# Performance work log

Measured on AMD Instinct MI355X. Metric: run time of the kernel, lower is better.

Reference implementation:

```python
import jax, jax.numpy as jnp
import numpy as np

N_NODES = 100000
N_EDGES = 1600000
IN_CH = 128
HID = 128
BN_EPS = 1e-5


def setup_inputs() -> dict:
    key = jax.random.key(0)
    ks = jax.random.split(key, 16)
    x = jax.random.normal(ks[0], (N_NODES, IN_CH), dtype=jnp.float32)
    edge_index = jax.random.randint(ks[1], (2, N_EDGES), 0, N_NODES, dtype=jnp.int32)
    edge_attr = jax.random.uniform(ks[2], (N_EDGES,), dtype=jnp.float32)
    def glorot(k, fan_in, fan_out):
        s = jnp.sqrt(6.0 / (fan_in + fan_out))
        return jax.random.uniform(k, (fan_in, fan_out), dtype=jnp.float32, minval=-s, maxval=s)
    W1 = glorot(ks[3], IN_CH, HID)
    b1 = jnp.zeros((HID,), jnp.float32)
    gamma1 = jnp.ones((HID,), jnp.float32)
    beta1 = jnp.zeros((HID,), jnp.float32)
    W2 = glorot(ks[4], HID, HID)
    b2 = jnp.zeros((HID,), jnp.float32)
    gamma2 = jnp.ones((HID,), jnp.float32)
    beta2 = jnp.zeros((HID,), jnp.float32)
    W3 = glorot(ks[5], HID, 1)
    b3 = jnp.zeros((1,), jnp.float32)
    return {"x": x, "edge_index": edge_index, "edge_attr": edge_attr,
            "W1": W1, "b1": b1, "gamma1": gamma1, "beta1": beta1,
            "W2": W2, "b2": b2, "gamma2": gamma2, "beta2": beta2,
            "W3": W3, "b3": b3}


def _gcn_norm(edge_index, edge_weight, num_nodes):
    # PyG gcn_norm with add_self_loops=True, self-loop weight 1.0
    sl = jnp.arange(num_nodes, dtype=edge_index.dtype)
    row = jnp.concatenate([edge_index[0], sl])  # source
    col = jnp.concatenate([edge_index[1], sl])  # target
    w = jnp.concatenate([edge_weight, jnp.ones((num_nodes,), edge_weight.dtype)])
    deg = jax.ops.segment_sum(w, col, num_segments=num_nodes)
    dinv = jnp.where(deg > 0, jax.lax.rsqrt(jnp.maximum(deg, 1e-30)), 0.0)
    norm = dinv[row] * w * dinv[col]
    return row, col, norm


def _gcn_conv(x, W, b, row, col, norm, num_nodes):
    xw = x @ W                       # [N, out]
    msg = xw[row] * norm[:, None]    # gather + scale, [E+N, out]
    out = jax.ops.segment_sum(msg, col, num_segments=num_nodes)  # scatter-add
    return out + b


def _batchnorm(x, gamma, beta):
    mean = jnp.mean(x, axis=0)
    var = jnp.mean(jnp.square(x - mean), axis=0)  # biased var (torch BN)
    return (x - mean) * jax.lax.rsqrt(var + BN_EPS) * gamma + beta


def reference(x, edge_index, edge_attr, W1, b1, gamma1, beta1, W2, b2, gamma2, beta2, W3, b3):
    n = x.shape[0]
    row, col, norm = _gcn_norm(edge_index, edge_attr, n)
    h = _gcn_conv(x, W1, b1, row, col, norm, n)
    h = jax.nn.relu(_batchnorm(h, gamma1, beta1))  # dropout = identity (eval)
    h = _gcn_conv(h, W2, b2, row, col, norm, n)
    h = jax.nn.relu(_batchnorm(h, gamma2, beta2))
    out = _gcn_conv(h, W3, b3, row, col, norm, n)  # [N, 1]
    return out
```

## Files before the change

### kernel.cpp

```cpp
#include <hip/hip_runtime.h>
#include <hip/hip_bf16.h>


#define HID 128
#define BN_EPS 1e-5f
#define BK 64

typedef __attribute__((ext_vector_type(8))) short bf16x8;
typedef __attribute__((ext_vector_type(4))) float f32x4;

static inline size_t alignup(size_t x){ return (x + 255) & ~(size_t)255; }


__global__ void k_initcur(int* cursor, int n){
  int i = blockIdx.x*256 + threadIdx.x;
  if (i < n) cursor[i] = 0;
}

__global__ void k_fill_direct(const int* __restrict__ ei, const float* __restrict__ attr,
                              int* __restrict__ cursor, int2* __restrict__ csr, int E){
  int e = blockIdx.x*256 + threadIdx.x;
  if (e >= E) return;
  int src = ei[e];
  int dst = ei[E + e];
  int pos = atomicAdd(&cursor[dst], 1);
  if (pos < BK)
    csr[(size_t)dst*BK + pos] = make_int2(src, __float_as_int(attr[e]));
}

__global__ __launch_bounds__(256) void k_degdinv(const int2* __restrict__ csr,
    const int* __restrict__ cursor, float* __restrict__ dinv, int N){
  int node = blockIdx.x*32 + (threadIdx.x >> 3);
  int l = threadIdx.x & 7;
  if (node >= N) return;
  int m = min(cursor[node], BK);
  float s = 0.f;
  for (int j = l; j < m; j += 8)
    s += __int_as_float(csr[(size_t)node*BK + j].y);
  s += __shfl_xor(s, 1, 8);
  s += __shfl_xor(s, 2, 8);
  s += __shfl_xor(s, 4, 8);
  if (l == 0) dinv[node] = 1.0f / sqrtf(1.0f + s);
}

__global__ __launch_bounds__(256) void k_wfin(int2* __restrict__ csr,
    const int* __restrict__ cursor, const float* __restrict__ dinv, int N){
  int node = blockIdx.x*32 + (threadIdx.x >> 3);
  int l = threadIdx.x & 7;
  if (node >= N) return;
  int m = min(cursor[node], BK);
  float di = dinv[node];
  for (int j = l; j < m; j += 8){
    int2 t = csr[(size_t)node*BK + j];
    float w = dinv[t.x] * __int_as_float(t.y) * di;
    csr[(size_t)node*BK + j] = make_int2(t.x, __float_as_int(w));
  }
}


static __device__ inline uint2 pack_bf16x4(float4 a){
  __hip_bfloat162 lo = __float22bfloat162_rn({a.x, a.y});
  __hip_bfloat162 hi = __float22bfloat162_rn({a.z, a.w});
  uint2 r;
  r.x = *(unsigned int*)&lo;
  r.y = *(unsigned int*)&hi;
  return r;
}

static __device__ inline unsigned short bfbits(float v){
  __hip_bfloat16 h = __float2bfloat16(v);
  return *(unsigned short*)&h;
}

__global__ void k_wtprep(const float* __restrict__ Wg, unsigned short* __restrict__ WTg){
  int idx = blockIdx.x*256 + threadIdx.x;
  int k   = idx >> 7;
  int col = idx & 127;
  WTg[(size_t)col*128 + k] = bfbits(Wg[(size_t)k*128 + col]);
}

template<bool BN>
__device__ inline void gemm_body(const float* __restrict__ A,
    const unsigned short* __restrict__ WTg, const float* __restrict__ coef,
    unsigned int* __restrict__ C, int n, int bid){
  int lane = threadIdx.x & 63;
  int wv4  = threadIdx.x >> 6;
  int l16  = lane & 15;
  int kg   = lane >> 4;
  int row_base = bid*128 + wv4*32;
  int nm1 = n - 1;
  int a0row = min(row_base + l16,      nm1);
  int a1row = min(row_base + 16 + l16, nm1);

  f32x4 acc[2][8] = {};
  #pragma unroll
  for (int k0 = 0; k0 < 128; k0 += 32){
    int k = k0 + kg*8;
    float4 lo0 = *(const float4*)(A + (size_t)a0row*HID + k);
    float4 hi0 = *(const float4*)(A + (size_t)a0row*HID + k + 4);
    float4 lo1 = *(const float4*)(A + (size_t)a1row*HID + k);
    float4 hi1 = *(const float4*)(A + (size_t)a1row*HID + k + 4);
    if (BN){
      float4 sca = *(const float4*)(coef + k);
      float4 scb = *(const float4*)(coef + k + 4);
      float4 sha = *(const float4*)(coef + 128 + k);
      float4 shb = *(const float4*)(coef + 128 + k + 4);
      lo0.x = fmaxf(fmaf(lo0.x, sca.x, sha.x), 0.f);
      lo0.y = fmaxf(fmaf(lo0.y, sca.y, sha.y), 0.f);
      lo0.z = fmaxf(fmaf(lo0.z, sca.z, sha.z), 0.f);
      lo0.w = fmaxf(fmaf(lo0.w, sca.w, sha.w), 0.f);
      hi0.x = fmaxf(fmaf(hi0.x, scb.x, shb.x), 0.f);
      hi0.y = fmaxf(fmaf(hi0.y, scb.y, shb.y), 0.f);
      hi0.z = fmaxf(fmaf(hi0.z, scb.z, shb.z), 0.f);
      hi0.w = fmaxf(fmaf(hi0.w, scb.w, shb.w), 0.f);
      lo1.x = fmaxf(fmaf(lo1.x, sca.x, sha.x), 0.f);
      lo1.y = fmaxf(fmaf(lo1.y, sca.y, sha.y), 0.f);
      lo1.z = fmaxf(fmaf(lo1.z, sca.z, sha.z), 0.f);
      lo1.w = fmaxf(fmaf(lo1.w, sca.w, sha.w), 0.f);
      hi1.x = fmaxf(fmaf(hi1.x, scb.x, shb.x), 0.f);
      hi1.y = fmaxf(fmaf(hi1.y, scb.y, shb.y), 0.f);
      hi1.z = fmaxf(fmaf(hi1.z, scb.z, shb.z), 0.f);
      hi1.w = fmaxf(fmaf(hi1.w, scb.w, shb.w), 0.f);
    }
    union { bf16x8 v; uint2 u[2]; } a0c, a1c;
    a0c.u[0] = pack_bf16x4(lo0); a0c.u[1] = pack_bf16x4(hi0);
    a1c.u[0] = pack_bf16x4(lo1); a1c.u[1] = pack_bf16x4(hi1);
    bf16x8 a0 = a0c.v, a1 = a1c.v;
    #pragma unroll
    for (int ct = 0; ct < 8; ++ct){
      int col = ct*16 + l16;
      bf16x8 b = *(const bf16x8*)(WTg + (size_t)col*128 + k);
      acc[0][ct] = __builtin_amdgcn_mfma_f32_16x16x32_bf16(a0, b, acc[0][ct], 0,0,0);
      acc[1][ct] = __builtin_amdgcn_mfma_f32_16x16x32_bf16(a1, b, acc[1][ct], 0,0,0);
    }
  }

  #pragma unroll
  for (int rt = 0; rt < 2; ++rt){
    int growb = row_base + rt*16 + kg*4;
    #pragma unroll
    for (int ct = 0; ct < 8; ++ct){
      #pragma unroll
      for (int r = 0; r < 4; ++r){
        float v = acc[rt][ct][r];
        float o = __shfl_xor(v, 1);
        if (!(lane & 1)){
          int grow = growb + r;
          if (grow < n){
            __hip_bfloat162 p2 = __float22bfloat162_rn({v, o});
            C[(size_t)grow*64 + ct*8 + (l16 >> 1)] = *(unsigned int*)&p2;
          }
        }
      }
    }
  }
}

__global__ __launch_bounds__(256) void k_gemm_mfma(const float* __restrict__ A,
    const unsigned short* __restrict__ WTg,
    unsigned int* __restrict__ C, int n){
  gemm_body<false>(A, WTg, nullptr, C, n, blockIdx.x);
}

__global__ __launch_bounds__(256) void k_gemm_mfma_bn(const float* __restrict__ A,
    const unsigned short* __restrict__ WTg, const float* __restrict__ coef,
    unsigned int* __restrict__ C, int n){
  gemm_body<true>(A, WTg, coef, C, n, blockIdx.x);
}


static __device__ inline float2 bf16pair(unsigned int u){
  __hip_bfloat162 h = *(__hip_bfloat162*)&u;
  return __bfloat1622float2(h);
}

struct Acc8 { float a0,a1,a2,a3,a4,a5,a6,a7; };

static __device__ inline void fma8(Acc8& a, uint4 v, float wt){
  float2 p0 = bf16pair(v.x), p1 = bf16pair(v.y);
  float2 p2 = bf16pair(v.z), p3 = bf16pair(v.w);
  a.a0 = fmaf(wt, p0.x, a.a0); a.a1 = fmaf(wt, p0.y, a.a1);
  a.a2 = fmaf(wt, p1.x, a.a2); a.a3 = fmaf(wt, p1.y, a.a3);
  a.a4 = fmaf(wt, p2.x, a.a4); a.a5 = fmaf(wt, p2.y, a.a5);
  a.a6 = fmaf(wt, p3.x, a.a6); a.a7 = fmaf(wt, p3.y, a.a7);
}

__global__ __launch_bounds__(256) void k_gather128(const unsigned int* __restrict__ xwb,
    const int2* __restrict__ csr, const int* __restrict__ cursor,
    const float* __restrict__ dinv, const float* __restrict__ bias,
    float* __restrict__ out, int n){
  int node = blockIdx.x*4 + (threadIdx.x >> 6);
  int lane = threadIdx.x & 63;
  if (node >= n) return;
  int l16 = lane & 15;
  int eg  = lane >> 4;
  size_t base = (size_t)node*BK;
  int m = min(cursor[node], BK);
  Acc8 a = {0,0,0,0,0,0,0,0};
  if (eg == 0){
    float di = dinv[node];
    float sw = di * di;
    uint4 sv = *(const uint4*)(xwb + (size_t)node*64 + l16*4);
    float4 b0 = *(const float4*)(bias + l16*8);
    float4 b1 = *(const float4*)(bias + l16*8 + 4);
    a.a0 = b0.x; a.a1 = b0.y; a.a2 = b0.z; a.a3 = b0.w;
    a.a4 = b1.x; a.a5 = b1.y; a.a6 = b1.z; a.a7 = b1.w;
    fma8(a, sv, sw);
  }
  int j = eg;
  for (; j + 4 < m; j += 8){
    int2 ea = csr[base + j];
    int2 eb = csr[base + j + 4];
    uint4 va = *(const uint4*)(xwb + (size_t)ea.x*64 + l16*4);
    uint4 vb = *(const uint4*)(xwb + (size_t)eb.x*64 + l16*4);
    fma8(a, va, __int_as_float(ea.y));
    fma8(a, vb, __int_as_float(eb.y));
  }
  if (j < m){
    int2 ea = csr[base + j];
    uint4 va = *(const uint4*)(xwb + (size_t)ea.x*64 + l16*4);
    fma8(a, va, __int_as_float(ea.y));
  }
  a.a0 += __shfl_xor(a.a0, 16); a.a1 += __shfl_xor(a.a1, 16);
  a.a2 += __shfl_xor(a.a2, 16); a.a3 += __shfl_xor(a.a3, 16);
  a.a4 += __shfl_xor(a.a4, 16); a.a5 += __shfl_xor(a.a5, 16);
  a.a6 += __shfl_xor(a.a6, 16); a.a7 += __shfl_xor(a.a7, 16);
  a.a0 += __shfl_xor(a.a0, 32); a.a1 += __shfl_xor(a.a1, 32);
  a.a2 += __shfl_xor(a.a2, 32); a.a3 += __shfl_xor(a.a3, 32);
  a.a4 += __shfl_xor(a.a4, 32); a.a5 += __shfl_xor(a.a5, 32);
  a.a6 += __shfl_xor(a.a6, 32); a.a7 += __shfl_xor(a.a7, 32);
  if (eg == 0){
    float4 r0; r0.x=a.a0; r0.y=a.a1; r0.z=a.a2; r0.w=a.a3;
    float4 r1; r1.x=a.a4; r1.y=a.a5; r1.z=a.a6; r1.w=a.a7;
    *(float4*)(out + (size_t)node*HID + l16*8)     = r0;
    *(float4*)(out + (size_t)node*HID + l16*8 + 4) = r1;
  }
}

__global__ __launch_bounds__(256) void k_bnstats(const float* __restrict__ h,
                                                 float* stats, int n){
  __shared__ float ls[256], lq[256];
  int c = threadIdx.x & 127;
  int r0 = blockIdx.x*2 + (threadIdx.x >> 7);
  float s = 0.f, q = 0.f;
  for (int r = r0; r < n; r += gridDim.x*2){
    float v = h[(size_t)r*HID + c];
    s += v;
    q = fmaf(v, v, q);
  }
  ls[threadIdx.x] = s; lq[threadIdx.x] = q;
  __syncthreads();
  if (threadIdx.x < 128){
    s = ls[threadIdx.x] + ls[threadIdx.x + 128];
    q = lq[threadIdx.x] + lq[threadIdx.x + 128];
    atomicAdd(&stats[c], s);
    atomicAdd(&stats[128 + c], q);
  }
}

__global__ void k_bnfin(const float* __restrict__ stats, const float* __restrict__ gamma,
                        const float* __restrict__ beta, float* coef, int n){
  int c = threadIdx.x;
  float inv_n = 1.0f / (float)n;
  float mean = stats[c] * inv_n;
  float var = fmaxf(stats[128 + c] * inv_n - mean*mean, 0.f);
  float sc = gamma[c] / sqrtf(var + BN_EPS);
  coef[c] = sc;
  coef[128 + c] = fmaf(-mean, sc, beta[c]);
}

__global__ __launch_bounds__(256) void k_dotW3(const float* __restrict__ h,
    const float* __restrict__ coef, const float* __restrict__ W3,
    float* __restrict__ xw3, int n){
  int lane = threadIdx.x & 31;
  int row = blockIdx.x*8 + (threadIdx.x >> 5);
  if (row >= n) return;
  float4 v  = *(const float4*)(h + (size_t)row*HID + lane*4);
  float4 sc = *(const float4*)(coef + lane*4);
  float4 sh = *(const float4*)(coef + 128 + lane*4);
  float4 w  = *(const float4*)(W3 + lane*4);
  float acc = fmaxf(fmaf(v.x, sc.x, sh.x), 0.f) * w.x
            + fmaxf(fmaf(v.y, sc.y, sh.y), 0.f) * w.y
            + fmaxf(fmaf(v.z, sc.z, sh.z), 0.f) * w.z
            + fmaxf(fmaf(v.w, sc.w, sh.w), 0.f) * w.w;
  #pragma unroll
  for (int m = 1; m < 32; m <<= 1) acc += __shfl_xor(acc, m, 32);
  if (lane == 0) xw3[row] = acc;
}

__global__ void k_gather1(const float* __restrict__ xw3, const int2* __restrict__ csr,
    const int* __restrict__ cursor, const float* __restrict__ dinv,
    const float* __restrict__ b3, float* __restrict__ out, int n){
  int i = blockIdx.x*256 + threadIdx.x;
  if (i >= n) return;
  float di = dinv[i];
  float acc = fmaf(di*di, xw3[i], b3[0]);
  size_t base = (size_t)i*BK;
  int m = min(cursor[i], BK);
  for (int j = 0; j < m; ++j){
    int2 e = csr[base + j];
    acc = fmaf(__int_as_float(e.y), xw3[e.x], acc);
  }
  out[i] = acc;
}

extern "C" void kernel_launch(void* const* d_in, const int* in_sizes, int n_in,
                              void* d_out, int out_size, void* d_ws, size_t ws_size,
                              hipStream_t stream){
  const float* x    = (const float*)d_in[0];
  const int*   ei   = (const int*)  d_in[1];
  const float* attr = (const float*)d_in[2];
  const float* W1   = (const float*)d_in[3];
  const float* b1   = (const float*)d_in[4];
  const float* g1   = (const float*)d_in[5];
  const float* be1  = (const float*)d_in[6];
  const float* W2   = (const float*)d_in[7];
  const float* b2   = (const float*)d_in[8];
  const float* g2   = (const float*)d_in[9];
  const float* be2  = (const float*)d_in[10];
  const float* W3   = (const float*)d_in[11];
  const float* b3   = (const float*)d_in[12];
  float* out = (float*)d_out;

  const int N = in_sizes[0] / HID;
  const int E = in_sizes[2];

  char* w = (char*)d_ws;
  auto take = [&](size_t bytes) -> char* { char* p = w; w += alignup(bytes); return p; };
  int*   cursor = (int*)  take((size_t)N*4);
  float* dinv   = (float*)take((size_t)N*4);
  float* stats  = (float*)take(256*4);
  float* coef1  = (float*)take(256*4);
  float* coef2  = (float*)take(256*4);
  unsigned short* wt1 = (unsigned short*)take(128*128*2);
  unsigned short* wt2 = (unsigned short*)take(128*128*2);
  int2*  csr    = (int2*) take((size_t)N*BK*8);
  float* xw3    = (float*)take((size_t)N*4);
  unsigned int* bufA = (unsigned int*)take((size_t)N*64*4);
  float* bufB   = (float*)take((size_t)N*HID*4);
  (void)ws_size; (void)n_in; (void)out_size;

  int nbN = (N + 255)/256;
  int nbE = (E + 255)/256;
  int nbG = (N + 127)/128;
  int nb8 = (N + 31)/32;

  k_initcur    <<<nbN, 256, 0, stream>>>(cursor, N);
  k_wtprep     <<<64,  256, 0, stream>>>(W1, wt1);
  k_wtprep     <<<64,  256, 0, stream>>>(W2, wt2);
  k_fill_direct<<<nbE, 256, 0, stream>>>(ei, attr, cursor, csr, E);
  k_gemm_mfma  <<<nbG, 256, 0, stream>>>(x, wt1, bufA, N);
  k_degdinv    <<<nb8, 256, 0, stream>>>(csr, cursor, dinv, N);
  k_wfin       <<<nb8, 256, 0, stream>>>(csr, cursor, dinv, N);

  k_gather128  <<<(N+3)/4, 256, 0, stream>>>(bufA, csr, cursor, dinv, b1, bufB, N);
  hipMemsetAsync(stats, 0, 256*4, stream);
  k_bnstats    <<<512, 256, 0, stream>>>(bufB, stats, N);
  k_bnfin      <<<1, 128, 0, stream>>>(stats, g1, be1, coef1, N);

  k_gemm_mfma_bn<<<nbG, 256, 0, stream>>>(bufB, wt2, coef1, bufA, N);
  k_gather128  <<<(N+3)/4, 256, 0, stream>>>(bufA, csr, cursor, dinv, b2, bufB, N);
  hipMemsetAsync(stats, 0, 256*4, stream);
  k_bnstats    <<<512, 256, 0, stream>>>(bufB, stats, N);
  k_bnfin      <<<1, 128, 0, stream>>>(stats, g2, be2, coef2, N);

  k_dotW3      <<<(N+7)/8, 256, 0, stream>>>(bufB, coef2, W3, xw3, N);
  k_gather1    <<<nbN, 256, 0, stream>>>(xw3, csr, cursor, dinv, b3, out, N);
}
```

Before: 449.4 us.

## Store aggregated hidden activations in bf16 and unroll gather loop further

The gather kernel now writes its per-node aggregated output as packed bf16 instead of fp32. BN stats, the second GEMM (with fused BN+ReLU) and the W3 dot all read the bf16 buffer, which halves the memory traffic of those passes. The gather loop is also unrolled to four edges per iteration, so more independent loads are in flight. The cost is extra rounding of pre-BatchNorm activations, which could shift the statistics and the final accuracy slightly.

```diff
diff --git a/kernel.cpp b/kernel.cpp
--- a/kernel.cpp
+++ b/kernel.cpp
@@ -58,12 +58,20 @@
 }
 
 
+static __device__ inline float2 bf16pair(unsigned int u){
+  __hip_bfloat162 h = *(__hip_bfloat162*)&u;
+  return __bfloat1622float2(h);
+}
+
+static __device__ inline unsigned int packpair(float x, float y){
+  __hip_bfloat162 p = __float22bfloat162_rn({x, y});
+  return *(unsigned int*)&p;
+}
+
 static __device__ inline uint2 pack_bf16x4(float4 a){
-  __hip_bfloat162 lo = __float22bfloat162_rn({a.x, a.y});
-  __hip_bfloat162 hi = __float22bfloat162_rn({a.z, a.w});
   uint2 r;
-  r.x = *(unsigned int*)&lo;
-  r.y = *(unsigned int*)&hi;
+  r.x = packpair(a.x, a.y);
+  r.y = packpair(a.z, a.w);
   return r;
 }
 
@@ -79,8 +87,8 @@
   WTg[(size_t)col*128 + k] = bfbits(Wg[(size_t)k*128 + col]);
 }
 
-template<bool BN>
-__device__ inline void gemm_body(const float* __restrict__ A,
+template<bool BN, bool AB16>
+__device__ inline void gemm_body(const void* __restrict__ Av,
     const unsigned short* __restrict__ WTg, const float* __restrict__ coef,
     unsigned int* __restrict__ C, int n, int bid){
   int lane = threadIdx.x & 63;
@@ -96,36 +104,51 @@
   #pragma unroll
   for (int k0 = 0; k0 < 128; k0 += 32){
     int k = k0 + kg*8;
-    float4 lo0 = *(const float4*)(A + (size_t)a0row*HID + k);
-    float4 hi0 = *(const float4*)(A + (size_t)a0row*HID + k + 4);
-    float4 lo1 = *(const float4*)(A + (size_t)a1row*HID + k);
-    float4 hi1 = *(const float4*)(A + (size_t)a1row*HID + k + 4);
+    float4 sca, scb, sha, shb;
     if (BN){
-      float4 sca = *(const float4*)(coef + k);
-      float4 scb = *(const float4*)(coef + k + 4);
-      float4 sha = *(const float4*)(coef + 128 + k);
-      float4 shb = *(const float4*)(coef + 128 + k + 4);
-      lo0.x = fmaxf(fmaf(lo0.x, sca.x, sha.x), 0.f);
-      lo0.y = fmaxf(fmaf(lo0.y, sca.y, sha.y), 0.f);
-      lo0.z = fmaxf(fmaf(lo0.z, sca.z, sha.z), 0.f);
-      lo0.w = fmaxf(fmaf(lo0.w, sca.w, sha.w), 0.f);
-      hi0.x = fmaxf(fmaf(hi0.x, scb.x, shb.x), 0.f);
-      hi0.y = fmaxf(fmaf(hi0.y, scb.y, shb.y), 0.f);
-      hi0.z = fmaxf(fmaf(hi0.z, scb.z, shb.z), 0.f);
-      hi0.w = fmaxf(fmaf(hi0.w, scb.w, shb.w), 0.f);
-      lo1.x = fmaxf(fmaf(lo1.x, sca.x, sha.x), 0.f);
-      lo1.y = fmaxf(fmaf(lo1.y, sca.y, sha.y), 0.f);
-      lo1.z = fmaxf(fmaf(lo1.z, sca.z, sha.z), 0.f);
-      lo1.w = fmaxf(fmaf(lo1.w, sca.w, sha.w), 0.f);
-      hi1.x = fmaxf(fmaf(hi1.x, scb.x, shb.x), 0.f);
-      hi1.y = fmaxf(fmaf(hi1.y, scb.y, shb.y), 0.f);
-      hi1.z = fmaxf(fmaf(hi1.z, scb.z, shb.z), 0.f);
-      hi1.w = fmaxf(fmaf(hi1.w, scb.w, shb.w), 0.f);
+      sca = *(const float4*)(coef + k);
+      scb = *(const float4*)(coef + k + 4);
+      sha = *(const float4*)(coef + 128 + k);
+      shb = *(const float4*)(coef + 128 + k + 4);
     }
-    union { bf16x8 v; uint2 u[2]; } a0c, a1c;
-    a0c.u[0] = pack_bf16x4(lo0); a0c.u[1] = pack_bf16x4(hi0);
-    a1c.u[0] = pack_bf16x4(lo1); a1c.u[1] = pack_bf16x4(hi1);
-    bf16x8 a0 = a0c.v, a1 = a1c.v;
+    bf16x8 a0, a1;
+    if constexpr (AB16){
+      const unsigned int* A = (const unsigned int*)Av;
+      uint4 u0 = *(const uint4*)(A + (size_t)a0row*64 + (k >> 1));
+      uint4 u1 = *(const uint4*)(A + (size_t)a1row*64 + (k >> 1));
+      #pragma unroll
+      for (int half = 0; half < 2; ++half){
+        uint4 u = half ? u1 : u0;
+        float2 p0 = bf16pair(u.x), p1 = bf16pair(u.y);
+        float2 p2 = bf16pair(u.z), p3 = bf16pair(u.w);
+        if (BN){
+          p0.x = fmaxf(fmaf(p0.x, sca.x, sha.x), 0.f);
+          p0.y = fmaxf(fmaf(p0.y, sca.y, sha.y), 0.f);
+          p1.x = fmaxf(fmaf(p1.x, sca.z, sha.z), 0.f);
+          p1.y = fmaxf(fmaf(p1.y, sca.w, sha.w), 0.f);
+          p2.x = fmaxf(fmaf(p2.x, scb.x, shb.x), 0.f);
+          p2.y = fmaxf(fmaf(p2.y, scb.y, shb.y), 0.f);
+          p3.x = fmaxf(fmaf(p3.x, scb.z, shb.z), 0.f);
+          p3.y = fmaxf(fmaf(p3.y, scb.w, shb.w), 0.f);
+        }
+        union { bf16x8 v; unsigned int u[4]; } c;
+        c.u[0] = packpair(p0.x, p0.y);
+        c.u[1] = packpair(p1.x, p1.y);
+        c.u[2] = packpair(p2.x, p2.y);
+        c.u[3] = packpair(p3.x, p3.y);
+        if (half) a1 = c.v; else a0 = c.v;
+      }
+    } else {
+      const float* A = (const float*)Av;
+      float4 lo0 = *(const float4*)(A + (size_t)a0row*HID + k);
+      float4 hi0 = *(const float4*)(A + (size_t)a0row*HID + k + 4);
+      float4 lo1 = *(const float4*)(A + (size_t)a1row*HID + k);
+      float4 hi1 = *(const float4*)(A + (size_t)a1row*HID + k + 4);
+      union { bf16x8 v; uint2 u[2]; } a0c, a1c;
+      a0c.u[0] = pack_bf16x4(lo0); a0c.u[1] = pack_bf16x4(hi0);
+      a1c.u[0] = pack_bf16x4(lo1); a1c.u[1] = pack_bf16x4(hi1);
+      a0 = a0c.v; a1 = a1c.v;
+    }
     #pragma unroll
     for (int ct = 0; ct < 8; ++ct){
       int col = ct*16 + l16;
@@ -147,8 +170,7 @@
         if (!(lane & 1)){
           int grow = growb + r;
           if (grow < n){
-            __hip_bfloat162 p2 = __float22bfloat162_rn({v, o});
-            C[(size_t)grow*64 + ct*8 + (l16 >> 1)] = *(unsigned int*)&p2;
+            C[(size_t)grow*64 + ct*8 + (l16 >> 1)] = packpair(v, o);
           }
         }
       }
@@ -159,20 +181,15 @@
 __global__ __launch_bounds__(256) void k_gemm_mfma(const float* __restrict__ A,
     const unsigned short* __restrict__ WTg,
     unsigned int* __restrict__ C, int n){
-  gemm_body<false>(A, WTg, nullptr, C, n, blockIdx.x);
-}
-
-__global__ __launch_bounds__(256) void k_gemm_mfma_bn(const float* __restrict__ A,
+  gemm_body<false,false>(A, WTg, nullptr, C, n, blockIdx.x);
+}
+
+__global__ __launch_bounds__(256) void k_gemm_mfma_bn16(const unsigned int* __restrict__ A,
     const unsigned short* __restrict__ WTg, const float* __restrict__ coef,
     unsigned int* __restrict__ C, int n){
-  gemm_body<true>(A, WTg, coef, C, n, blockIdx.x);
-}
-
-
-static __device__ inline float2 bf16pair(unsigned int u){
-  __hip_bfloat162 h = *(__hip_bfloat162*)&u;
-  return __bfloat1622float2(h);
-}
+  gemm_body<true,true>(A, WTg, coef, C, n, blockIdx.x);
+}
+
 
 struct Acc8 { float a0,a1,a2,a3,a4,a5,a6,a7; };
 
@@ -188,7 +205,7 @@
 __global__ __launch_bounds__(256) void k_gather128(const unsigned int* __restrict__ xwb,
     const int2* __restrict__ csr, const int* __restrict__ cursor,
     const float* __restrict__ dinv, const float* __restrict__ bias,
-    float* __restrict__ out, int n){
+    unsigned int* __restrict__ out, int n){
   int node = blockIdx.x*4 + (threadIdx.x >> 6);
   int lane = threadIdx.x & 63;
   if (node >= n) return;
@@ -208,15 +225,21 @@
     fma8(a, sv, sw);
   }
   int j = eg;
-  for (; j + 4 < m; j += 8){
-    int2 ea = csr[base + j];
-    int2 eb = csr[base + j + 4];
-    uint4 va = *(const uint4*)(xwb + (size_t)ea.x*64 + l16*4);
-    uint4 vb = *(const uint4*)(xwb + (size_t)eb.x*64 + l16*4);
-    fma8(a, va, __int_as_float(ea.y));
-    fma8(a, vb, __int_as_float(eb.y));
-  }
-  if (j < m){
+  for (; j + 12 < m; j += 16){
+    int2 e0 = csr[base + j];
+    int2 e1 = csr[base + j + 4];
+    int2 e2 = csr[base + j + 8];
+    int2 e3 = csr[base + j + 12];
+    uint4 v0 = *(const uint4*)(xwb + (size_t)e0.x*64 + l16*4);
+    uint4 v1 = *(const uint4*)(xwb + (size_t)e1.x*64 + l16*4);
+    uint4 v2 = *(const uint4*)(xwb + (size_t)e2.x*64 + l16*4);
+    uint4 v3 = *(const uint4*)(xwb + (size_t)e3.x*64 + l16*4);
+    fma8(a, v0, __int_as_float(e0.y));
+    fma8(a, v1, __int_as_float(e1.y));
+    fma8(a, v2, __int_as_float(e2.y));
+    fma8(a, v3, __int_as_float(e3.y));
+  }
+  for (; j < m; j += 4){
     int2 ea = csr[base + j];
     uint4 va = *(const uint4*)(xwb + (size_t)ea.x*64 + l16*4);
     fma8(a, va, __int_as_float(ea.y));
@@ -230,31 +253,38 @@
   a.a4 += __shfl_xor(a.a4, 32); a.a5 += __shfl_xor(a.a5, 32);
   a.a6 += __shfl_xor(a.a6, 32); a.a7 += __shfl_xor(a.a7, 32);
   if (eg == 0){
-    float4 r0; r0.x=a.a0; r0.y=a.a1; r0.z=a.a2; r0.w=a.a3;
-    float4 r1; r1.x=a.a4; r1.y=a.a5; r1.z=a.a6; r1.w=a.a7;
-    *(float4*)(out + (size_t)node*HID + l16*8)     = r0;
-    *(float4*)(out + (size_t)node*HID + l16*8 + 4) = r1;
-  }
-}
-
-__global__ __launch_bounds__(256) void k_bnstats(const float* __restrict__ h,
+    uint4 r;
+    r.x = packpair(a.a0, a.a1);
+    r.y = packpair(a.a2, a.a3);
+    r.z = packpair(a.a4, a.a5);
+    r.w = packpair(a.a6, a.a7);
+    *(uint4*)(out + (size_t)node*64 + l16*4) = r;
+  }
+}
+
+__global__ __launch_bounds__(256) void k_bnstats(const unsigned int* __restrict__ h,
                                                  float* stats, int n){
-  __shared__ float ls[256], lq[256];
-  int c = threadIdx.x & 127;
-  int r0 = blockIdx.x*2 + (threadIdx.x >> 7);
-  float s = 0.f, q = 0.f;
-  for (int r = r0; r < n; r += gridDim.x*2){
-    float v = h[(size_t)r*HID + c];
-    s += v;
-    q = fmaf(v, v, q);
-  }
-  ls[threadIdx.x] = s; lq[threadIdx.x] = q;
+  __shared__ float ls0[256], ls1[256], lq0[256], lq1[256];
+  int p  = threadIdx.x & 63;
+  int r0 = blockIdx.x*4 + (threadIdx.x >> 6);
+  float s0=0.f, s1=0.f, q0=0.f, q1=0.f;
+  for (int r = r0; r < n; r += gridDim.x*4){
+    float2 v = bf16pair(h[(size_t)r*64 + p]);
+    s0 += v.x; q0 = fmaf(v.x, v.x, q0);
+    s1 += v.y; q1 = fmaf(v.y, v.y, q1);
+  }
+  ls0[threadIdx.x]=s0; ls1[threadIdx.x]=s1; lq0[threadIdx.x]=q0; lq1[threadIdx.x]=q1;
   __syncthreads();
-  if (threadIdx.x < 128){
-    s = ls[threadIdx.x] + ls[threadIdx.x + 128];
-    q = lq[threadIdx.x] + lq[threadIdx.x + 128];
-    atomicAdd(&stats[c], s);
-    atomicAdd(&stats[128 + c], q);
+  if (threadIdx.x < 64){
+    int t = threadIdx.x;
+    s0 = ls0[t]+ls0[t+64]+ls0[t+128]+ls0[t+192];
+    s1 = ls1[t]+ls1[t+64]+ls1[t+128]+ls1[t+192];
+    q0 = lq0[t]+lq0[t+64]+lq0[t+128]+lq0[t+192];
+    q1 = lq1[t]+lq1[t+64]+lq1[t+128]+lq1[t+192];
+    atomicAdd(&stats[2*t],       s0);
+    atomicAdd(&stats[2*t+1],     s1);
+    atomicAdd(&stats[128+2*t],   q0);
+    atomicAdd(&stats[128+2*t+1], q1);
   }
 }
 
@@ -269,22 +299,23 @@
   coef[128 + c] = fmaf(-mean, sc, beta[c]);
 }
 
-__global__ __launch_bounds__(256) void k_dotW3(const float* __restrict__ h,
+__global__ __launch_bounds__(256) void k_dotW3(const unsigned int* __restrict__ h,
     const float* __restrict__ coef, const float* __restrict__ W3,
     float* __restrict__ xw3, int n){
   int lane = threadIdx.x & 31;
   int row = blockIdx.x*8 + (threadIdx.x >> 5);
   if (row >= n) return;
-  float4 v  = *(const float4*)(h + (size_t)row*HID + lane*4);
+  uint2 u = *(const uint2*)(h + (size_t)row*64 + lane*2);
+  float2 va = bf16pair(u.x), vb = bf16pair(u.y);
   float4 sc = *(const float4*)(coef + lane*4);
   float4 sh = *(const float4*)(coef + 128 + lane*4);
   float4 w  = *(const float4*)(W3 + lane*4);
-  float acc = fmaxf(fmaf(v.x, sc.x, sh.x), 0.f) * w.x
-            + fmaxf(fmaf(v.y, sc.y, sh.y), 0.f) * w.y
-            + fmaxf(fmaf(v.z, sc.z, sh.z), 0.f) * w.z
-            + fmaxf(fmaf(v.w, sc.w, sh.w), 0.f) * w.w;
+  float acc = fmaxf(fmaf(va.x, sc.x, sh.x), 0.f) * w.x
+            + fmaxf(fmaf(va.y, sc.y, sh.y), 0.f) * w.y
+            + fmaxf(fmaf(vb.x, sc.z, sh.z), 0.f) * w.z
+            + fmaxf(fmaf(vb.y, sc.w, sh.w), 0.f) * w.w;
   #pragma unroll
-  for (int m = 1; m < 32; m <<= 1) acc += __shfl_xor(acc, m, 32);
+  for (int mm = 1; mm < 32; mm <<= 1) acc += __shfl_xor(acc, mm, 32);
   if (lane == 0) xw3[row] = acc;
 }
 
@@ -337,7 +368,7 @@
   int2*  csr    = (int2*) take((size_t)N*BK*8);
   float* xw3    = (float*)take((size_t)N*4);
   unsigned int* bufA = (unsigned int*)take((size_t)N*64*4);
-  float* bufB   = (float*)take((size_t)N*HID*4);
+  unsigned int* bufB = (unsigned int*)take((size_t)N*64*4);
   (void)ws_size; (void)n_in; (void)out_size;
 
   int nbN = (N + 255)/256;
@@ -358,7 +389,7 @@
   k_bnstats    <<<512, 256, 0, stream>>>(bufB, stats, N);
   k_bnfin      <<<1, 128, 0, stream>>>(stats, g1, be1, coef1, N);
 
-  k_gemm_mfma_bn<<<nbG, 256, 0, stream>>>(bufB, wt2, coef1, bufA, N);
+  k_gemm_mfma_bn16<<<nbG, 256, 0, stream>>>(bufB, wt2, coef1, bufA, N);
   k_gather128  <<<(N+3)/4, 256, 0, stream>>>(bufA, csr, cursor, dinv, b2, bufB, N);
   hipMemsetAsync(stats, 0, 256*4, stream);
   k_bnstats    <<<512, 256, 0, stream>>>(bufB, stats, N);
```

Result: no change. 447.9 us (-0.3%).
